# Optimization experiments

Hardware: AMD Instinct MI355X
Metric: run time of the kernel (lower is better)

Reference implementation:

```python
import jax, jax.numpy as jnp
import numpy as np

CHAMFER_WEIGHT = 1.0
REG_WEIGHT = 0.1


def setup_inputs() -> dict:
    key = jax.random.key(0)
    k1, k2, k3 = jax.random.split(key, 3)
    B, N, M, K = 16, 4096, 4096, 64
    return {
        "predicted_points": jax.random.normal(k1, (B, N, 3), dtype=jnp.float32),
        "ground_truth_points": jax.random.normal(k2, (B, M, 3), dtype=jnp.float32),
        "trans_feat": jax.random.normal(k3, (B, K, K), dtype=jnp.float32),
    }


def _chamfer(pred, target):
    # Euclidean (non-squared) pairwise distances, matching torch.cdist.
    # Gram trick avoids materializing [B,N,M,3].
    p2 = jnp.sum(pred * pred, axis=-1)          # [B,N]
    t2 = jnp.sum(target * target, axis=-1)      # [B,M]
    cross = jnp.einsum("bnd,bmd->bnm", pred, target)  # [B,N,M]
    d2 = p2[:, :, None] + t2[:, None, :] - 2.0 * cross
    dist = jnp.sqrt(jnp.maximum(d2, 0.0))       # [B,N,M]
    min1 = jnp.min(dist, axis=2)                # [B,N] pred -> nearest target
    min2 = jnp.min(dist, axis=1)                # [B,M] target -> nearest pred
    return jnp.mean(jnp.mean(min1, axis=1) + jnp.mean(min2, axis=1))


def _feature_transform_reg(trans):
    K = trans.shape[1]
    I = jnp.eye(K, dtype=trans.dtype)
    gram = jnp.einsum("bik,bjk->bij", trans, trans)  # trans @ trans^T
    # Frobenius norm per batch element, then mean over batch
    return jnp.mean(jnp.sqrt(jnp.sum((gram - I) ** 2, axis=(1, 2))))


def reference(predicted_points, ground_truth_points, trans_feat):
    chamfer = _chamfer(predicted_points, ground_truth_points)
    reg = _feature_transform_reg(trans_feat)
    return CHAMFER_WEIGHT * chamfer + REG_WEIGHT * reg
```

## Files before the change

### kernel.cpp

```cpp
#include <hip/hip_runtime.h>
#include <math.h>

#define BB 16
#define NN 4096
#define MM 4096
#define NSLICE 2
#define SLICE_COLS 2048
#define NJT (SLICE_COLS / 64)
#define ROWS_PER_WAVE 64
#define ROWS_PER_BLOCK 256
#define NROWS_TOTAL (2 * BB * NN)
#define NCHAMFER 1024
#define EPW 2176

typedef __attribute__((ext_vector_type(8))) short bf16x8;
typedef __attribute__((ext_vector_type(16))) float f32x16;

static __device__ inline unsigned short f2bf(float f) {
    unsigned int u = __float_as_uint(f);
    return (unsigned short)((u + 0x7FFFu + ((u >> 16) & 1u)) >> 16);
}
static __device__ inline bf16x8 bzero() {
    bf16x8 z;
    #pragma unroll
    for (int i = 0; i < 8; ++i) z[i] = 0;
    return z;
}
static __device__ inline f32x16 fzero16() {
    f32x16 z;
    #pragma unroll
    for (int i = 0; i < 16; ++i) z[i] = 0.f;
    return z;
}

#define MFMA32(Af, Bf, Cf) __builtin_amdgcn_mfma_f32_32x32x16_bf16(Af, Bf, Cf, 0, 0, 0)

__global__ __launch_bounds__(256, 4) void chamfer_min_kernel(
    const float* __restrict__ pred, const float* __restrict__ gt,
    const float* __restrict__ trans, float* __restrict__ wsmin,
    float* __restrict__ out)
{
    const int bx  = blockIdx.x;
    const int tid = threadIdx.x;

    if (bx >= NCHAMFER) {
        if (tid < 64) {
            const int b = bx - NCHAMFER;
            const int lane = tid;
            const int hi = lane >> 5, li = lane & 31;
            const float* T = trans + (size_t)b * 64 * 64;
            float fsum = 0.f;
            #pragma unroll
            for (int fi = 0; fi < 2; ++fi) {
                bf16x8 fa[4];
                #pragma unroll
                for (int s = 0; s < 4; ++s) {
                    const float* rp = T + (size_t)(fi * 32 + li) * 64 + s * 16 + hi * 8;
                    const float4 u0 = *(const float4*)rp;
                    const float4 u1 = *(const float4*)(rp + 4);
                    bf16x8 fr;
                    fr[0] = (short)f2bf(u0.x); fr[1] = (short)f2bf(u0.y);
                    fr[2] = (short)f2bf(u0.z); fr[3] = (short)f2bf(u0.w);
                    fr[4] = (short)f2bf(u1.x); fr[5] = (short)f2bf(u1.y);
                    fr[6] = (short)f2bf(u1.z); fr[7] = (short)f2bf(u1.w);
                    fa[s] = fr;
                }
                #pragma unroll
                for (int fj = 0; fj < 2; ++fj) {
                    f32x16 a = fzero16();
                    #pragma unroll
                    for (int s = 0; s < 4; ++s) {
                        const float* rp = T + (size_t)(fj * 32 + li) * 64 + s * 16 + hi * 8;
                        const float4 u0 = *(const float4*)rp;
                        const float4 u1 = *(const float4*)(rp + 4);
                        bf16x8 fr;
                        fr[0] = (short)f2bf(u0.x); fr[1] = (short)f2bf(u0.y);
                        fr[2] = (short)f2bf(u0.z); fr[3] = (short)f2bf(u0.w);
                        fr[4] = (short)f2bf(u1.x); fr[5] = (short)f2bf(u1.y);
                        fr[6] = (short)f2bf(u1.z); fr[7] = (short)f2bf(u1.w);
                        a = MFMA32(fa[s], fr, a);
                    }
                    #pragma unroll
                    for (int r = 0; r < 16; ++r) {
                        const int row = fi * 32 + (r & 3) + 8 * (r >> 2) + 4 * hi;
                        const int col = fj * 32 + li;
                        const float d = a[r] - ((row == col) ? 1.0f : 0.0f);
                        fsum = fmaf(d, d, fsum);
                    }
                }
            }
            #pragma unroll
            for (int off = 32; off > 0; off >>= 1)
                fsum += __shfl_down(fsum, off, 64);
            if (lane == 0)
                atomicAdd(out, (0.1f / (float)BB) * sqrtf(fsum));
        }
        return;
    }

    __shared__ __align__(16) float smem[4 * EPW];

    const int lane = tid & 63;
    const int w    = tid >> 6;
    const int li   = lane & 31;
    const int hi   = lane >> 5;
    const int tile   = bx & 15;
    const int mslice = (bx >> 4) & 1;
    const int b      = (bx >> 5) & 15;
    const int dir    = bx >> 9;
    const float* rows = dir ? gt : pred;
    const float* cols = dir ? pred : gt;
    const float* rb = rows + (size_t)b * NN * 3;
    const float* cb = cols + ((size_t)b * MM + (size_t)mslice * SLICE_COLS) * 3;

    const int rbase = tile * ROWS_PER_BLOCK + w * ROWS_PER_WAVE;
    bf16x8 A0 = bzero(), A1 = bzero();
    if (lane < 32) {
        #pragma unroll
        for (int f = 0; f < 2; ++f) {
            const float* rp = rb + (size_t)(rbase + f * 32 + li) * 3;
            const float px = rp[0], py = rp[1], pz = rp[2];
            const float p2 = px * px + py * py + pz * pz;
            bf16x8 fr = bzero();
            fr[0] = (short)f2bf(-2.f * px);
            fr[1] = (short)f2bf(-2.f * py);
            fr[2] = (short)f2bf(-2.f * pz);
            fr[3] = (short)f2bf(p2);
            fr[4] = (short)0x3F80;
            if (f == 0) A0 = fr; else A1 = fr;
        }
    }

    uint4* sB = (uint4*)smem;
    #pragma unroll
    for (int i = 0; i < SLICE_COLS / 512; ++i) {
        const int c0 = i * 512 + 2 * tid;
        const float2* sp = (const float2*)(cb + (size_t)c0 * 3);
        const float2 v0 = sp[0], v1 = sp[1], v2 = sp[2];
        const float t2a = v0.x * v0.x + v0.y * v0.y + v1.x * v1.x;
        const float t2b = v1.y * v1.y + v2.x * v2.x + v2.y * v2.y;
        uint4 pa, pb;
        pa.x = (unsigned)f2bf(v0.x) | ((unsigned)f2bf(v0.y) << 16);
        pa.y = (unsigned)f2bf(v1.x) | (0x3F80u << 16);
        pa.z = (unsigned)f2bf(t2a);
        pa.w = 0u;
        pb.x = (unsigned)f2bf(v1.y) | ((unsigned)f2bf(v2.x) << 16);
        pb.y = (unsigned)f2bf(v2.y) | (0x3F80u << 16);
        pb.z = (unsigned)f2bf(t2b);
        pb.w = 0u;
        sB[c0]     = pa;
        sB[c0 + 1] = pb;
    }
    __syncthreads();

    float mv0[16], mv1[16];
    #pragma unroll
    for (int r = 0; r < 16; ++r) { mv0[r] = 3.4e38f; mv1[r] = 3.4e38f; }

    const f32x16 Z = fzero16();
    const bf16x8* sBf = (const bf16x8*)smem;

    for (int jt = 0; jt < NJT; ++jt) {
        const bf16x8 c1 = sBf[jt * 64 + li];
        const bf16x8 c2 = sBf[jt * 64 + 32 + li];
        f32x16 a0 = MFMA32(A0, c1, Z);
        f32x16 a1 = MFMA32(A0, c2, Z);
        f32x16 a2 = MFMA32(A1, c1, Z);
        f32x16 a3 = MFMA32(A1, c2, Z);
        #pragma unroll
        for (int r = 0; r < 16; ++r)
            mv0[r] = fminf(fminf(a0[r], a1[r]), mv0[r]);
        #pragma unroll
        for (int r = 0; r < 16; ++r)
            mv1[r] = fminf(fminf(a2[r], a3[r]), mv1[r]);
    }

    __syncthreads();
    {
        float* wb = smem + w * EPW + li * 68;
        #pragma unroll
        for (int q = 0; q < 4; ++q) {
            const int rl = q * 8 + hi * 4;
            *(float4*)&wb[rl]      = make_float4(mv0[4*q], mv0[4*q+1], mv0[4*q+2], mv0[4*q+3]);
            *(float4*)&wb[rl + 32] = make_float4(mv1[4*q], mv1[4*q+1], mv1[4*q+2], mv1[4*q+3]);
        }
    }
    __syncthreads();

    const int wsrc = tid >> 6, rl = tid & 63;
    const float* rb2 = smem + wsrc * EPW + rl;
    float m = 3.4e38f;
    #pragma unroll
    for (int c = 0; c < 32; ++c) m = fminf(m, rb2[c * 68]);
    wsmin[(size_t)mslice * NROWS_TOTAL + (size_t)(dir * BB + b) * NN
          + tile * ROWS_PER_BLOCK + tid] = m;
}

__global__ __launch_bounds__(256) void chamfer_finish_kernel(
    const float* __restrict__ wsmin, float* __restrict__ out)
{
    const int tid = threadIdx.x;
    const int g = blockIdx.x * 256 + tid;
    const float v = fminf(wsmin[g], wsmin[NROWS_TOTAL + g]);
    float d = sqrtf(fmaxf(v, 0.0f));
    #pragma unroll
    for (int off = 32; off > 0; off >>= 1)
        d += __shfl_down(d, off, 64);
    __shared__ float ssum[4];
    if ((tid & 63) == 0) ssum[tid >> 6] = d;
    __syncthreads();
    if (tid == 0) {
        const float s = ssum[0] + ssum[1] + ssum[2] + ssum[3];
        atomicAdd(out, s * (1.0f / ((float)BB * (float)NN)));
    }
}

extern "C" void kernel_launch(void* const* d_in, const int* in_sizes, int n_in,
                              void* d_out, int out_size, void* d_ws, size_t ws_size,
                              hipStream_t stream)
{
    const float* pred  = (const float*)d_in[0];
    const float* gt    = (const float*)d_in[1];
    const float* trans = (const float*)d_in[2];
    float* out = (float*)d_out;
    float* wsmin = (float*)d_ws;

    hipMemsetAsync(out, 0, sizeof(float), stream);
    chamfer_min_kernel<<<dim3(NCHAMFER + BB), dim3(256), 0, stream>>>(
        pred, gt, trans, wsmin, out);
    chamfer_finish_kernel<<<dim3(NROWS_TOTAL / 256), dim3(256), 0, stream>>>(
        wsmin, out);
}
```

Measured before the change: 33.18 us.

## Compute both chamfer directions from one distance tile via column atomicMin

Each distance tile is now computed once and reduced along both rows and columns. This halves the chamfer blocks and drops the reversed-direction pass. Column minima are gathered per block with shared-memory atomicMin on float bits offset by +1, so negative values still order correctly. They are written to workspace, and the finish kernel combines the 16 row tiles. The regularizer path also reuses its converted bf16 fragments instead of reloading them, and launch bounds move to 2 blocks per CU. The cost is extra min work and LDS atomics in the inner loop, plus higher register and LDS pressure.

```diff
diff --git a/kernel.cpp b/kernel.cpp
--- a/kernel.cpp
+++ b/kernel.cpp
@@ -7,11 +7,10 @@
 #define NSLICE 2
 #define SLICE_COLS 2048
 #define NJT (SLICE_COLS / 64)
-#define ROWS_PER_WAVE 64
 #define ROWS_PER_BLOCK 256
-#define NROWS_TOTAL (2 * BB * NN)
-#define NCHAMFER 1024
+#define NCHAMFER 512
 #define EPW 2176
+#define WSCOL_OFF (BB * NSLICE * NN)
 
 typedef __attribute__((ext_vector_type(8))) short bf16x8;
 typedef __attribute__((ext_vector_type(16))) float f32x16;
@@ -35,9 +34,9 @@
 
 #define MFMA32(Af, Bf, Cf) __builtin_amdgcn_mfma_f32_32x32x16_bf16(Af, Bf, Cf, 0, 0, 0)
 
-__global__ __launch_bounds__(256, 4) void chamfer_min_kernel(
+__global__ __launch_bounds__(256, 2) void chamfer_min_kernel(
     const float* __restrict__ pred, const float* __restrict__ gt,
-    const float* __restrict__ trans, float* __restrict__ wsmin,
+    const float* __restrict__ trans, float* __restrict__ ws,
     float* __restrict__ out)
 {
     const int bx  = blockIdx.x;
@@ -49,13 +48,12 @@
             const int lane = tid;
             const int hi = lane >> 5, li = lane & 31;
             const float* T = trans + (size_t)b * 64 * 64;
-            float fsum = 0.f;
+            bf16x8 frag[2][4];
             #pragma unroll
-            for (int fi = 0; fi < 2; ++fi) {
-                bf16x8 fa[4];
+            for (int h = 0; h < 2; ++h)
                 #pragma unroll
                 for (int s = 0; s < 4; ++s) {
-                    const float* rp = T + (size_t)(fi * 32 + li) * 64 + s * 16 + hi * 8;
+                    const float* rp = T + (size_t)(h * 32 + li) * 64 + s * 16 + hi * 8;
                     const float4 u0 = *(const float4*)rp;
                     const float4 u1 = *(const float4*)(rp + 4);
                     bf16x8 fr;
@@ -63,23 +61,17 @@
                     fr[2] = (short)f2bf(u0.z); fr[3] = (short)f2bf(u0.w);
                     fr[4] = (short)f2bf(u1.x); fr[5] = (short)f2bf(u1.y);
                     fr[6] = (short)f2bf(u1.z); fr[7] = (short)f2bf(u1.w);
-                    fa[s] = fr;
+                    frag[h][s] = fr;
                 }
+            float fsum = 0.f;
+            #pragma unroll
+            for (int fi = 0; fi < 2; ++fi)
                 #pragma unroll
                 for (int fj = 0; fj < 2; ++fj) {
                     f32x16 a = fzero16();
                     #pragma unroll
-                    for (int s = 0; s < 4; ++s) {
-                        const float* rp = T + (size_t)(fj * 32 + li) * 64 + s * 16 + hi * 8;
-                        const float4 u0 = *(const float4*)rp;
-                        const float4 u1 = *(const float4*)(rp + 4);
-                        bf16x8 fr;
-                        fr[0] = (short)f2bf(u0.x); fr[1] = (short)f2bf(u0.y);
-                        fr[2] = (short)f2bf(u0.z); fr[3] = (short)f2bf(u0.w);
-                        fr[4] = (short)f2bf(u1.x); fr[5] = (short)f2bf(u1.y);
-                        fr[6] = (short)f2bf(u1.z); fr[7] = (short)f2bf(u1.w);
-                        a = MFMA32(fa[s], fr, a);
-                    }
+                    for (int s = 0; s < 4; ++s)
+                        a = MFMA32(frag[fi][s], frag[fj][s], a);
                     #pragma unroll
                     for (int r = 0; r < 16; ++r) {
                         const int row = fi * 32 + (r & 3) + 8 * (r >> 2) + 4 * hi;
@@ -88,7 +80,6 @@
                         fsum = fmaf(d, d, fsum);
                     }
                 }
-            }
             #pragma unroll
             for (int off = 32; off > 0; off >>= 1)
                 fsum += __shfl_down(fsum, off, 64);
@@ -98,7 +89,8 @@
         return;
     }
 
-    __shared__ __align__(16) float smem[4 * EPW];
+    __shared__ __align__(16) float smem[8704];
+    __shared__ unsigned int colmin[SLICE_COLS];
 
     const int lane = tid & 63;
     const int w    = tid >> 6;
@@ -106,14 +98,11 @@
     const int hi   = lane >> 5;
     const int tile   = bx & 15;
     const int mslice = (bx >> 4) & 1;
-    const int b      = (bx >> 5) & 15;
-    const int dir    = bx >> 9;
-    const float* rows = dir ? gt : pred;
-    const float* cols = dir ? pred : gt;
-    const float* rb = rows + (size_t)b * NN * 3;
-    const float* cb = cols + ((size_t)b * MM + (size_t)mslice * SLICE_COLS) * 3;
-
-    const int rbase = tile * ROWS_PER_BLOCK + w * ROWS_PER_WAVE;
+    const int b      = bx >> 5;
+    const float* rb = pred + (size_t)b * NN * 3;
+    const float* cb = gt + ((size_t)b * MM + (size_t)mslice * SLICE_COLS) * 3;
+
+    const int rbase = tile * ROWS_PER_BLOCK + w * 64;
     bf16x8 A0 = bzero(), A1 = bzero();
     if (lane < 32) {
         #pragma unroll
@@ -151,6 +140,9 @@
         sB[c0]     = pa;
         sB[c0 + 1] = pb;
     }
+    #pragma unroll
+    for (int i = 0; i < SLICE_COLS / 256; ++i)
+        colmin[i * 256 + tid] = 0x7F7FFFFFu;
     __syncthreads();
 
     float mv0[16], mv1[16];
@@ -160,6 +152,7 @@
     const f32x16 Z = fzero16();
     const bf16x8* sBf = (const bf16x8*)smem;
 
+    #pragma unroll 2
     for (int jt = 0; jt < NJT; ++jt) {
         const bf16x8 c1 = sBf[jt * 64 + li];
         const bf16x8 c2 = sBf[jt * 64 + 32 + li];
@@ -173,6 +166,18 @@
         #pragma unroll
         for (int r = 0; r < 16; ++r)
             mv1[r] = fminf(fminf(a2[r], a3[r]), mv1[r]);
+        float tA = fminf(a0[0], a0[1]);
+        #pragma unroll
+        for (int i = 1; i < 8; ++i) tA = fminf(fminf(a0[2*i], a0[2*i+1]), tA);
+        #pragma unroll
+        for (int i = 0; i < 8; ++i) tA = fminf(fminf(a2[2*i], a2[2*i+1]), tA);
+        float tB = fminf(a1[0], a1[1]);
+        #pragma unroll
+        for (int i = 1; i < 8; ++i) tB = fminf(fminf(a1[2*i], a1[2*i+1]), tB);
+        #pragma unroll
+        for (int i = 0; i < 8; ++i) tB = fminf(fminf(a3[2*i], a3[2*i+1]), tB);
+        atomicMin(&colmin[jt * 64 + li],      __float_as_uint(tA + 1.0f));
+        atomicMin(&colmin[jt * 64 + 32 + li], __float_as_uint(tB + 1.0f));
     }
 
     __syncthreads();
@@ -187,21 +192,45 @@
     }
     __syncthreads();
 
-    const int wsrc = tid >> 6, rl = tid & 63;
-    const float* rb2 = smem + wsrc * EPW + rl;
-    float m = 3.4e38f;
-    #pragma unroll
-    for (int c = 0; c < 32; ++c) m = fminf(m, rb2[c * 68]);
-    wsmin[(size_t)mslice * NROWS_TOTAL + (size_t)(dir * BB + b) * NN
-          + tile * ROWS_PER_BLOCK + tid] = m;
+    {
+        const int wsrc = tid >> 6, rl = tid & 63;
+        const float* rb2 = smem + wsrc * EPW + rl;
+        float m = 3.4e38f;
+        #pragma unroll
+        for (int c = 0; c < 32; ++c) m = fminf(m, rb2[c * 68]);
+        ws[((size_t)b * NSLICE + mslice) * NN + tile * ROWS_PER_BLOCK + tid] = m;
+    }
+    {
+        float* wc = ws + WSCOL_OFF
+                  + (((size_t)b * 16 + tile) * NSLICE + mslice) * SLICE_COLS;
+        #pragma unroll
+        for (int i = 0; i < SLICE_COLS / 256; ++i) {
+            const int c = i * 256 + tid;
+            wc[c] = __uint_as_float(colmin[c]) - 1.0f;
+        }
+    }
 }
 
 __global__ __launch_bounds__(256) void chamfer_finish_kernel(
-    const float* __restrict__ wsmin, float* __restrict__ out)
+    const float* __restrict__ ws, float* __restrict__ out)
 {
     const int tid = threadIdx.x;
     const int g = blockIdx.x * 256 + tid;
-    const float v = fminf(wsmin[g], wsmin[NROWS_TOTAL + g]);
+    float v;
+    if (g < BB * NN) {
+        const int b = g >> 12, n = g & (NN - 1);
+        const float* p = ws + ((size_t)b * NSLICE) * NN + n;
+        v = fminf(p[0], p[NN]);
+    } else {
+        const int h = g - BB * NN;
+        const int b = h >> 12, m = h & (MM - 1);
+        const int s = m >> 11, c = m & (SLICE_COLS - 1);
+        const float* p = ws + WSCOL_OFF + (((size_t)b * 16) * NSLICE + s) * SLICE_COLS + c;
+        v = p[0];
+        #pragma unroll
+        for (int t = 1; t < 16; ++t)
+            v = fminf(v, p[(size_t)t * NSLICE * SLICE_COLS]);
+    }
     float d = sqrtf(fmaxf(v, 0.0f));
     #pragma unroll
     for (int off = 32; off > 0; off >>= 1)
@@ -223,11 +252,11 @@
     const float* gt    = (const float*)d_in[1];
     const float* trans = (const float*)d_in[2];
     float* out = (float*)d_out;
-    float* wsmin = (float*)d_ws;
+    float* ws = (float*)d_ws;
 
     hipMemsetAsync(out, 0, sizeof(float), stream);
     chamfer_min_kernel<<<dim3(NCHAMFER + BB), dim3(256), 0, stream>>>(
-        pred, gt, trans, wsmin, out);
-    chamfer_finish_kernel<<<dim3(NROWS_TOTAL / 256), dim3(256), 0, stream>>>(
-        wsmin, out);
-}
+        pred, gt, trans, ws, out);
+    chamfer_finish_kernel<<<dim3((2 * BB * NN) / 256), dim3(256), 0, stream>>>(
+        ws, out);
+}
```

Result: no change. 33.16 us (-0.1%).
